# Kernel tuning notes

Measured on AMD Instinct MI355X. Metric: run time of the kernel, lower is better.

## Reference

```python
import math
import jax, jax.numpy as jnp
import numpy as np

DIM = 1280
NUM_HEADS = 16
HEAD_DIM = DIM // NUM_HEADS  # 80
N_SEG = 8
SEG_LEN = 1024
TOTAL = N_SEG * SEG_LEN  # 8192


def setup_inputs() -> dict:
    key = jax.random.key(0)
    ks = jax.random.split(key, 6)
    hidden_states = jax.random.normal(ks[0], (TOTAL, DIM), dtype=jnp.float32)
    # equal-length packed segments (8 images x 1024 patches)
    cu_seqlens = jnp.arange(N_SEG + 1, dtype=jnp.int32) * SEG_LEN
    rotary_pos_emb = jax.random.uniform(ks[1], (TOTAL, HEAD_DIM // 2), dtype=jnp.float32) * (2.0 * math.pi)
    s = 0.02
    qkv_w = jax.random.normal(ks[2], (DIM, 3 * DIM), dtype=jnp.float32) * s
    qkv_b = jnp.zeros((3 * DIM,), dtype=jnp.float32)
    proj_w = jax.random.normal(ks[3], (DIM, DIM), dtype=jnp.float32) * s
    proj_b = jnp.zeros((DIM,), dtype=jnp.float32)
    return {
        "hidden_states": hidden_states,
        "rotary_pos_emb": rotary_pos_emb,
        "qkv_w": qkv_w,
        "qkv_b": qkv_b,
        "proj_w": proj_w,
        "proj_b": proj_b,
        "cu_seqlens": cu_seqlens,
    }


def _rotate_half(x):
    d = x.shape[-1] // 2
    return jnp.concatenate([-x[..., d:], x[..., :d]], axis=-1)


def _apply_rope(t, freqs):
    # t: [S, H, D] ; freqs: [S, D/2]
    orig = t.dtype
    tf = t.astype(jnp.float32)
    cos = jnp.tile(jnp.cos(freqs), (1, 2))[:, None, :].astype(jnp.float32)  # [S,1,D]
    sin = jnp.tile(jnp.sin(freqs), (1, 2))[:, None, :].astype(jnp.float32)
    return (tf * cos + _rotate_half(tf) * sin).astype(orig)


def reference(hidden_states, rotary_pos_emb, qkv_w, qkv_b, proj_w, proj_b, cu_seqlens):
    S, dim = hidden_states.shape
    H, D = NUM_HEADS, HEAD_DIM
    n_seg = cu_seqlens.shape[0] - 1  # static
    L = S // n_seg  # equal-length segments

    qkv = hidden_states @ qkv_w + qkv_b            # [S, 3*dim]
    qkv = qkv.reshape(S, 3, H, D)
    q, k, v = qkv[:, 0], qkv[:, 1], qkv[:, 2]      # [S, H, D]

    q = _apply_rope(q, rotary_pos_emb)
    k = _apply_rope(k, rotary_pos_emb)

    # block-diagonal (per-segment) attention, vectorized over segments
    qs = q.reshape(n_seg, L, H, D).transpose(0, 2, 1, 3)  # [G,H,L,D]
    ks = k.reshape(n_seg, L, H, D).transpose(0, 2, 1, 3)
    vs = v.reshape(n_seg, L, H, D).transpose(0, 2, 1, 3)

    scale = 1.0 / math.sqrt(D)
    scores = jnp.einsum("ghld,ghmd->ghlm", qs, ks) * scale       # [G,H,L,L]
    probs = jax.nn.softmax(scores.astype(jnp.float32), axis=-1).astype(qs.dtype)
    out = jnp.einsum("ghlm,ghmd->ghld", probs, vs)               # [G,H,L,D]
    out = out.transpose(0, 2, 1, 3).reshape(S, H * D)            # [S, dim]
    return out @ proj_w + proj_b
```

## Files before the change

kernel.cpp:

```cpp
#include <hip/hip_runtime.h>
#include <hip/hip_bf16.h>
#include <math.h>

#define DIM 1280
#define NHEADS 16
#define HD 80
#define HDP 96
#define NSEG 8
#define SEGLEN 1024
#define TOTAL (NSEG*SEGLEN)

typedef unsigned short u16;
typedef __attribute__((ext_vector_type(8))) short bf16x8;
typedef __attribute__((ext_vector_type(4))) float f32x4;

#define QSCALE 0.16129841766598387f

__device__ __forceinline__ u16 f2b(float f) {
    union { float f; unsigned int i; } v; v.f = f;
    unsigned int x = v.i;
    unsigned int r = x + 0x7FFFu + ((x >> 16) & 1u);
    return (u16)(r >> 16);
}
__device__ __forceinline__ float b2f(u16 u) {
    union { unsigned int i; float f; } v; v.i = ((unsigned int)u) << 16;
    return v.f;
}
__device__ __forceinline__ void gload16(const u16* g, u16* l) {
    __builtin_amdgcn_global_load_lds(
        (const __attribute__((address_space(1))) unsigned int*)g,
        (__attribute__((address_space(3))) unsigned int*)l, 16, 0, 0);
}
__device__ __forceinline__ unsigned int cvt_pk_bf16(float lo, float hi) {
    unsigned int r;
    asm("v_cvt_pk_bf16_f32 %0, %1, %2" : "=v"(r) : "v"(lo), "v"(hi));
    return r;
}

__global__ __launch_bounds__(256) void cvt_f32_bf16(const float* __restrict__ in,
                                                    u16* __restrict__ out, int n4) {
    int i = blockIdx.x * 256 + threadIdx.x;
    if (i >= n4) return;
    float4 a = ((const float4*)in)[i];
    u16 o[4] = { f2b(a.x), f2b(a.y), f2b(a.z), f2b(a.w) };
    *(ulong1*)&out[i*4] = *(ulong1*)o;
}

__global__ __launch_bounds__(256) void cvtT_w(const float* __restrict__ in,
                                              u16* __restrict__ out, int K, int N) {
    __shared__ float t[32][33];
    const int kb = blockIdx.x * 32, nb = blockIdx.y * 32;
    const int tx = threadIdx.x & 31, ty = threadIdx.x >> 5;
    #pragma unroll
    for (int i = 0; i < 4; ++i) {
        int r = i*8 + ty;
        t[r][tx] = in[(size_t)(kb + r)*N + nb + tx];
    }
    __syncthreads();
    #pragma unroll
    for (int i = 0; i < 4; ++i) {
        int n = i*8 + ty;
        out[(size_t)(nb + n)*K + kb + tx] = f2b(t[tx][n]);
    }
}

__global__ __launch_bounds__(256) void ctab_build(const float* __restrict__ rp,
                                                  float2* __restrict__ cs) {
    int i = blockIdx.x * 256 + threadIdx.x;
    if (i >= TOTAL*40) return;
    float s, c;
    sincosf(rp[i], &s, &c);
    cs[i] = make_float2(c, s);
}

template<int MODE>
__global__ __launch_bounds__(512, 2) void gemm8p(
    const u16* __restrict__ A, const u16* __restrict__ BT,
    const float* __restrict__ bias,
    float* __restrict__ Cf, u16* __restrict__ qo, u16* __restrict__ ko,
    u16* __restrict__ vo, int M, int N, int K, int nbx)
{
    __shared__ u16 sA[2][256*64];
    __shared__ u16 sB[2][256*64];

    const int tid = threadIdx.x;
    const int w = tid >> 6, l = tid & 63;
    const int lq = l & 15, lg = l >> 4;
    const int wm = w >> 2, wn = w & 3;

    const int nwg = gridDim.x;
    const int q8 = nwg >> 3;
    const int id = blockIdx.x;
    const int id2 = (id & 7) * q8 + (id >> 3);
    const int bx = id2 % nbx, by = id2 / nbx;
    const int brow = by * 256, bcol = bx * 256;

    const int rlo  = w*8 + (l >> 3);
    const int srcc = (l & 7) ^ ((l >> 3) & 7);
    const size_t aBase = (size_t)(brow + rlo)*K + srcc*8;
    const size_t bBase = (size_t)(bcol + rlo)*K + srcc*8;

    const int cx0 = (0 + lg) ^ (lq & 7);
    const int cx1 = (4 + lg) ^ (lq & 7);

    f32x4 acc[8][4] = {};
    const int NT = K >> 6;

    u16* cA = &sA[0][0]; u16* cB = &sB[0][0];
    u16* nA = &sA[1][0]; u16* nB = &sB[1][0];

    #pragma unroll
    for (int ci = 0; ci < 4; ++ci) {
        gload16(A  + aBase + (size_t)(ci*64)*K, &cA[(ci*512 + w*64)*8]);
        gload16(BT + bBase + (size_t)(ci*64)*K, &cB[(ci*512 + w*64)*8]);
    }
    asm volatile("s_waitcnt vmcnt(0)" ::: "memory");
    __builtin_amdgcn_s_barrier();

    for (int t = 0; t < NT; ++t) {
        const bool pf = (t + 1 < NT);
        const int kb = (t + 1) << 6;
        bf16x8 af[4], bf[4];

        if (pf) {
            #pragma unroll
            for (int ci = 0; ci < 4; ++ci) {
                gload16(A  + aBase + (size_t)(ci*64)*K + kb, &nA[(ci*512 + w*64)*8]);
                gload16(BT + bBase + (size_t)(ci*64)*K + kb, &nB[(ci*512 + w*64)*8]);
            }
        }

        #pragma unroll
        for (int n = 0; n < 4; ++n)
            bf[n] = *(const bf16x8*)&cB[(wn*64 + n*16 + lq)*64 + cx0*8];
        #pragma unroll
        for (int mi = 0; mi < 4; ++mi)
            af[mi] = *(const bf16x8*)&cA[(wm*128 + mi*16 + lq)*64 + cx0*8];
        __builtin_amdgcn_s_barrier();
        __builtin_amdgcn_s_setprio(1);
        #pragma unroll
        for (int mi = 0; mi < 4; ++mi)
            #pragma unroll
            for (int n = 0; n < 4; ++n)
                acc[mi][n] = __builtin_amdgcn_mfma_f32_16x16x32_bf16(af[mi], bf[n], acc[mi][n], 0, 0, 0);
        __builtin_amdgcn_s_setprio(0);
        __builtin_amdgcn_s_barrier();

        #pragma unroll
        for (int mi = 0; mi < 4; ++mi)
            af[mi] = *(const bf16x8*)&cA[(wm*128 + 64 + mi*16 + lq)*64 + cx0*8];
        __builtin_amdgcn_s_barrier();
        __builtin_amdgcn_s_setprio(1);
        #pragma unroll
        for (int mi = 0; mi < 4; ++mi)
            #pragma unroll
            for (int n = 0; n < 4; ++n)
                acc[4+mi][n] = __builtin_amdgcn_mfma_f32_16x16x32_bf16(af[mi], bf[n], acc[4+mi][n], 0, 0, 0);
        __builtin_amdgcn_s_setprio(0);
        __builtin_amdgcn_s_barrier();

        #pragma unroll
        for (int n = 0; n < 4; ++n)
            bf[n] = *(const bf16x8*)&cB[(wn*64 + n*16 + lq)*64 + cx1*8];
        #pragma unroll
        for (int mi = 0; mi < 4; ++mi)
            af[mi] = *(const bf16x8*)&cA[(wm*128 + mi*16 + lq)*64 + cx1*8];
        __builtin_amdgcn_s_barrier();
        __builtin_amdgcn_s_setprio(1);
        #pragma unroll
        for (int mi = 0; mi < 4; ++mi)
            #pragma unroll
            for (int n = 0; n < 4; ++n)
                acc[mi][n] = __builtin_amdgcn_mfma_f32_16x16x32_bf16(af[mi], bf[n], acc[mi][n], 0, 0, 0);
        __builtin_amdgcn_s_setprio(0);
        __builtin_amdgcn_s_barrier();

        #pragma unroll
        for (int mi = 0; mi < 4; ++mi)
            af[mi] = *(const bf16x8*)&cA[(wm*128 + 64 + mi*16 + lq)*64 + cx1*8];
        __builtin_amdgcn_s_barrier();
        __builtin_amdgcn_s_setprio(1);
        #pragma unroll
        for (int mi = 0; mi < 4; ++mi)
            #pragma unroll
            for (int n = 0; n < 4; ++n)
                acc[4+mi][n] = __builtin_amdgcn_mfma_f32_16x16x32_bf16(af[mi], bf[n], acc[4+mi][n], 0, 0, 0);
        __builtin_amdgcn_s_setprio(0);
        if (pf) asm volatile("s_waitcnt vmcnt(0)" ::: "memory");
        __builtin_amdgcn_s_barrier();

        u16* tA = cA; cA = nA; nA = tA;
        u16* tB = cB; cB = nB; nB = tB;
    }

    #pragma unroll
    for (int mf = 0; mf < 8; ++mf) {
        #pragma unroll
        for (int n = 0; n < 4; ++n) {
            const int col = bcol + wn*64 + n*16 + lq;
            const float bv = bias[col];
            #pragma unroll
            for (int r = 0; r < 4; ++r) {
                const int row = brow + wm*128 + mf*16 + lg*4 + r;
                float val = acc[mf][n][r] + bv;
                if (MODE == 0) {
                    Cf[(size_t)row*N + col] = val;
                } else {
                    int part = col / DIM, rem = col - part*DIM;
                    int hh = rem / HD, dd = rem - hh*HD;
                    int g = row >> 10, ll = row & 1023;
                    size_t tok = (size_t)((g*NHEADS + hh)*SEGLEN + ll);
                    if      (part == 0) qo[tok*HDP + dd] = f2b(val * QSCALE);
                    else if (part == 1) ko[tok*HDP + dd] = f2b(val);
                    else                vo[tok*HD  + dd] = f2b(val);
                }
            }
        }
    }
}

__global__ __launch_bounds__(256) void rope_pad2(u16* __restrict__ qb, u16* __restrict__ kb,
                                                 const float2* __restrict__ cs)
{
    int idx = blockIdx.x * 256 + threadIdx.x;
    int l = idx & 1023, h = (idx >> 10) & 15, g = idx >> 14;
    size_t base = ((size_t)((g*NHEADS + h)*SEGLEN + l)) * HDP;
    const float2* c0 = cs + (size_t)(g*SEGLEN + l) * 40;
    #pragma unroll
    for (int p = 0; p < 5; ++p) {
        float cv[8], sv[8];
        #pragma unroll
        for (int j2 = 0; j2 < 4; ++j2) {
            float4 f = ((const float4*)(c0 + p*8))[j2];
            cv[j2*2] = f.x; sv[j2*2] = f.y; cv[j2*2+1] = f.z; sv[j2*2+1] = f.w;
        }
        bf16x8 qlo = *(const bf16x8*)&qb[base + p*8];
        bf16x8 qhi = *(const bf16x8*)&qb[base + 40 + p*8];
        bf16x8 klo = *(const bf16x8*)&kb[base + p*8];
        bf16x8 khi = *(const bf16x8*)&kb[base + 40 + p*8];
        bf16x8 qlo2, qhi2, klo2, khi2;
        #pragma unroll
        for (int j = 0; j < 8; ++j) {
            float a  = b2f((u16)qlo[j]), b  = b2f((u16)qhi[j]);
            qlo2[j] = (short)f2b(a*cv[j]  - b*sv[j]);
            qhi2[j] = (short)f2b(b*cv[j]  + a*sv[j]);
            float ka = b2f((u16)klo[j]), kb2 = b2f((u16)khi[j]);
            klo2[j] = (short)f2b(ka*cv[j] - kb2*sv[j]);
            khi2[j] = (short)f2b(kb2*cv[j] + ka*sv[j]);
        }
        *(bf16x8*)&qb[base + p*8]      = qlo2;
        *(bf16x8*)&qb[base + 40 + p*8] = qhi2;
        *(bf16x8*)&kb[base + p*8]      = klo2;
        *(bf16x8*)&kb[base + 40 + p*8] = khi2;
    }
    bf16x8 z = {};
    *(bf16x8*)&qb[base + 80] = z; *(bf16x8*)&qb[base + 88] = z;
    *(bf16x8*)&kb[base + 80] = z; *(bf16x8*)&kb[base + 88] = z;
}

__global__ __launch_bounds__(256) void transpose_v(const u16* __restrict__ v,
                                                   u16* __restrict__ vt)
{
    __shared__ u16 sT[64][82];
    const int gh = blockIdx.y;
    const int st = blockIdx.x;
    const u16* src = v  + (size_t)gh*SEGLEN*HD + (size_t)st*64*HD;
    u16*       dst = vt + (size_t)gh*HD*SEGLEN + (size_t)st*64;
    const int tid = threadIdx.x;
    #pragma unroll
    for (int p = 0; p < 20; ++p) {
        int e = p*256 + tid;
        int r = e / 80, c = e - r*80;
        sT[r][c] = src[r*HD + c];
    }
    __syncthreads();
    #pragma unroll
    for (int p = 0; p < 20; ++p) {
        int e = p*256 + tid;
        int dd = e >> 6, s = e & 63;
        dst[(size_t)dd*SEGLEN + s] = sT[s][dd];
    }
}

__global__ __launch_bounds__(256) void attn_mfma(
    const u16* __restrict__ qb, const u16* __restrict__ kb,
    const u16* __restrict__ vt, u16* __restrict__ ob)
{
    const int qt = blockIdx.x;
    const int h  = blockIdx.y;
    const int g  = blockIdx.z;

    __shared__ u16 sK[64*HDP];
    __shared__ u16 sVT[80][72];
    __shared__ u16 sP[4][16][72];

    const int tid = threadIdx.x;
    const int w = tid >> 6, l = tid & 63;
    const int lq = l & 15, lg = l >> 4;

    const size_t gh = (size_t)(g*NHEADS + h);
    const u16* Qg  = qb + gh*SEGLEN*HDP + (size_t)qt*64*HDP;
    const u16* Kg  = kb + gh*SEGLEN*HDP;
    const u16* VTg = vt + gh*HD*SEGLEN;

    const int sig_l = l ^ ((l >> 3) & 7);
    int srow[3], scc[3];
    #pragma unroll
    for (int i = 0; i < 3; ++i) {
        int gi = (i*4 + w)*64 + sig_l;
        srow[i] = gi / 12;
        scc[i]  = gi % 12;
    }

    bf16x8 qf[3];
    #pragma unroll
    for (int s = 0; s < 3; ++s)
        qf[s] = *(const bf16x8*)(Qg + (size_t)(w*16 + lq)*HDP + s*32 + lg*8);

    float m = -1e30f, lse = 0.f;
    f32x4 Oc[5] = {};

    for (int kt = 0; kt < 16; ++kt) {
        __syncthreads();
        #pragma unroll
        for (int i = 0; i < 3; ++i)
            gload16(Kg + (size_t)(kt*64 + srow[i])*HDP + scc[i]*8, &sK[(i*4 + w)*512]);
        #pragma unroll
        for (int p = 0; p < 3; ++p) {
            int c = p*256 + tid;
            if (c < 640) {
                int dd = c >> 3, s8 = (c & 7)*8;
                *(bf16x8*)&sVT[dd][s8] =
                    *(const bf16x8*)(VTg + (size_t)dd*SEGLEN + kt*64 + s8);
            }
        }
        __syncthreads();

        f32x4 sf[4];
        #pragma unroll
        for (int fi = 0; fi < 4; ++fi) {
            f32x4 c = {0.f, 0.f, 0.f, 0.f};
            #pragma unroll
            for (int s = 0; s < 3; ++s) {
                int flat = (fi*16 + lq)*12 + s*4 + lg;
                int c6 = flat & 63;
                int lc = (flat & ~63) | (c6 ^ ((c6 >> 3) & 7));
                bf16x8 a = *(const bf16x8*)&sK[lc*8];
                c = __builtin_amdgcn_mfma_f32_16x16x32_bf16(a, qf[s], c, 0, 0, 0);
            }
            sf[fi] = c;
        }

        float sv[4][4];
        float rm = -1e30f;
        #pragma unroll
        for (int fi = 0; fi < 4; ++fi)
            #pragma unroll
            for (int r = 0; r < 4; ++r) {
                float x = sf[fi][r];
                sv[fi][r] = x;
                rm = fmaxf(rm, x);
            }
        rm = fmaxf(rm, __shfl_xor(rm, 16, 64));
        rm = fmaxf(rm, __shfl_xor(rm, 32, 64));

        if (__all(rm <= m + 8.0f)) {
            float psum = 0.f;
            #pragma unroll
            for (int fi = 0; fi < 4; ++fi)
                #pragma unroll
                for (int r = 0; r < 4; ++r) {
                    float p = exp2f(sv[fi][r] - m);
                    sv[fi][r] = p;
                    psum += p;
                }
            psum += __shfl_xor(psum, 16, 64);
            psum += __shfl_xor(psum, 32, 64);
            lse += psum;
        } else {
            float mnew = fmaxf(m, rm);
            float alpha = exp2f(m - mnew);
            float psum = 0.f;
            #pragma unroll
            for (int fi = 0; fi < 4; ++fi)
                #pragma unroll
                for (int r = 0; r < 4; ++r) {
                    float p = exp2f(sv[fi][r] - mnew);
                    sv[fi][r] = p;
                    psum += p;
                }
            psum += __shfl_xor(psum, 16, 64);
            psum += __shfl_xor(psum, 32, 64);
            lse = lse * alpha + psum;
            m = mnew;
            float a0 = __shfl(alpha, lg*4 + 0, 64);
            float a1 = __shfl(alpha, lg*4 + 1, 64);
            float a2 = __shfl(alpha, lg*4 + 2, 64);
            float a3 = __shfl(alpha, lg*4 + 3, 64);
            #pragma unroll
            for (int n = 0; n < 5; ++n) {
                Oc[n][0] *= a0; Oc[n][1] *= a1; Oc[n][2] *= a2; Oc[n][3] *= a3;
            }
        }

        #pragma unroll
        for (int fi = 0; fi < 4; ++fi) {
            uint2 val;
            val.x = cvt_pk_bf16(sv[fi][0], sv[fi][1]);
            val.y = cvt_pk_bf16(sv[fi][2], sv[fi][3]);
            *(uint2*)&sP[w][lq][fi*16 + lg*4] = val;
        }

        #pragma unroll
        for (int ks = 0; ks < 2; ++ks) {
            bf16x8 pa = *(const bf16x8*)&sP[w][lq][ks*32 + lg*8];
            #pragma unroll
            for (int n = 0; n < 5; ++n) {
                bf16x8 vb = *(const bf16x8*)&sVT[n*16 + lq][ks*32 + lg*8];
                Oc[n] = __builtin_amdgcn_mfma_f32_16x16x32_bf16(pa, vb, Oc[n], 0, 0, 0);
            }
        }
    }

    float inv = 1.f / lse;
    float i0 = __shfl(inv, lg*4 + 0, 64);
    float i1 = __shfl(inv, lg*4 + 1, 64);
    float i2 = __shfl(inv, lg*4 + 2, 64);
    float i3 = __shfl(inv, lg*4 + 3, 64);
    const float iv[4] = { i0, i1, i2, i3 };
    #pragma unroll
    for (int n = 0; n < 5; ++n) {
        #pragma unroll
        for (int r = 0; r < 4; ++r) {
            int tok = g*SEGLEN + qt*64 + w*16 + lg*4 + r;
            int col = h*HD + n*16 + lq;
            ob[(size_t)tok*DIM + col] = f2b(Oc[n][r] * iv[r]);
        }
    }
}

extern "C" void kernel_launch(void* const* d_in, const int* in_sizes, int n_in,
                              void* d_out, int out_size, void* d_ws, size_t ws_size,
                              hipStream_t stream) {
    const float* hs     = (const float*)d_in[0];
    const float* rope   = (const float*)d_in[1];
    const float* qkv_w  = (const float*)d_in[2];
    const float* qkv_b  = (const float*)d_in[3];
    const float* proj_w = (const float*)d_in[4];
    const float* proj_b = (const float*)d_in[5];

    char* ws = (char*)d_ws;
    u16* hsb    = (u16*)(ws);
    u16* wqkvt  = (u16*)(ws + 20971520);
    u16* wprojt = (u16*)(ws + 30801920);
    u16* qpad   = (u16*)(ws + 34078720);
    u16* kpad   = (u16*)(ws + 59244544);
    u16* vbuf   = (u16*)(ws + 84410368);
    u16* vtb    = (u16*)(ws + 105381888);
    u16* obb    = (u16*)(ws + 126353408);
    float2* ctab = (float2*)(ws + 126353408);

    cvt_f32_bf16<<<(TOTAL*DIM/4 + 255)/256, 256, 0, stream>>>(hs, hsb, TOTAL*DIM/4);
    cvtT_w<<<dim3(DIM/32, 3*DIM/32), 256, 0, stream>>>(qkv_w, wqkvt, DIM, 3*DIM);
    cvtT_w<<<dim3(DIM/32, DIM/32), 256, 0, stream>>>(proj_w, wprojt, DIM, DIM);
    ctab_build<<<(TOTAL*40 + 255)/256, 256, 0, stream>>>(rope, ctab);

    gemm8p<1><<<dim3((3*DIM/256) * (TOTAL/256)), 512, 0, stream>>>(
        hsb, wqkvt, qkv_b, nullptr, qpad, kpad, vbuf, TOTAL, 3*DIM, DIM, 3*DIM/256);

    rope_pad2<<<NSEG*NHEADS*SEGLEN/256, 256, 0, stream>>>(qpad, kpad, ctab);

    transpose_v<<<dim3(SEGLEN/64, NSEG*NHEADS), 256, 0, stream>>>(vbuf, vtb);

    attn_mfma<<<dim3(SEGLEN/64, NHEADS, NSEG), 256, 0, stream>>>(qpad, kpad, vtb, obb);

    gemm8p<0><<<dim3((DIM/256) * (TOTAL/256)), 512, 0, stream>>>(
        obb, wprojt, proj_b, (float*)d_out, nullptr, nullptr, nullptr, TOTAL, DIM, DIM, DIM/256);
}
```

Baseline: 478.8 us.

## Restructure GEMM pipeline, fuse V transpose, widen rope threads, double attention query tile

The GEMM now uses a depth-2 prefetch with partial vmcnt waits and far fewer barriers per K step, with K fixed at compile time. The QKV epilogue writes V directly in transposed layout, which removes the separate transpose kernel and its buffer. The rope kernel splits each row across six threads for more parallelism. Attention processes 128 queries per block (32 per wave), so each K/V tile loaded into shared memory is reused twice, at the cost of higher register pressure and half as many blocks.

Result: faster. 434.0 us (-9.4%).

```diff
diff --git a/kernel.cpp b/kernel.cpp
--- a/kernel.cpp
+++ b/kernel.cpp
@@ -74,12 +74,14 @@
 }
 
 template<int MODE>
-__global__ __launch_bounds__(512, 2) void gemm8p(
+__global__ __launch_bounds__(512, 2) void gemm_cv(
     const u16* __restrict__ A, const u16* __restrict__ BT,
     const float* __restrict__ bias,
     float* __restrict__ Cf, u16* __restrict__ qo, u16* __restrict__ ko,
-    u16* __restrict__ vo, int M, int N, int K, int nbx)
+    u16* __restrict__ vo, int M, int N, int nbx)
 {
+    const int K = 1280;
+    const int NT = 20;
     __shared__ u16 sA[2][256*64];
     __shared__ u16 sB[2][256*64];
 
@@ -104,7 +106,6 @@
     const int cx1 = (4 + lg) ^ (lq & 7);
 
     f32x4 acc[8][4] = {};
-    const int NT = K >> 6;
 
     u16* cA = &sA[0][0]; u16* cB = &sB[0][0];
     u16* nA = &sA[1][0]; u16* nB = &sB[1][0];
@@ -114,81 +115,51 @@
         gload16(A  + aBase + (size_t)(ci*64)*K, &cA[(ci*512 + w*64)*8]);
         gload16(BT + bBase + (size_t)(ci*64)*K, &cB[(ci*512 + w*64)*8]);
     }
-    asm volatile("s_waitcnt vmcnt(0)" ::: "memory");
-    __builtin_amdgcn_s_barrier();
-
+    #pragma unroll
+    for (int ci = 0; ci < 4; ++ci) {
+        gload16(A  + aBase + (size_t)(ci*64)*K + 64, &nA[(ci*512 + w*64)*8]);
+        gload16(BT + bBase + (size_t)(ci*64)*K + 64, &nB[(ci*512 + w*64)*8]);
+    }
+
+    #pragma unroll 2
     for (int t = 0; t < NT; ++t) {
-        const bool pf = (t + 1 < NT);
-        const int kb = (t + 1) << 6;
-        bf16x8 af[4], bf[4];
-
-        if (pf) {
+        if (t < NT - 1) asm volatile("s_waitcnt vmcnt(8)" ::: "memory");
+        else            asm volatile("s_waitcnt vmcnt(0)" ::: "memory");
+        __builtin_amdgcn_s_barrier();
+
+        #pragma unroll
+        for (int kh = 0; kh < 2; ++kh) {
+            const int cx = kh ? cx1 : cx0;
+            bf16x8 bf[4];
+            #pragma unroll
+            for (int n = 0; n < 4; ++n)
+                bf[n] = *(const bf16x8*)&cB[(wn*64 + n*16 + lq)*64 + cx*8];
+            #pragma unroll
+            for (int mh = 0; mh < 2; ++mh) {
+                bf16x8 af[4];
+                #pragma unroll
+                for (int mi = 0; mi < 4; ++mi)
+                    af[mi] = *(const bf16x8*)&cA[(wm*128 + mh*64 + mi*16 + lq)*64 + cx*8];
+                __builtin_amdgcn_s_setprio(1);
+                #pragma unroll
+                for (int mi = 0; mi < 4; ++mi)
+                    #pragma unroll
+                    for (int n = 0; n < 4; ++n)
+                        acc[mh*4 + mi][n] = __builtin_amdgcn_mfma_f32_16x16x32_bf16(
+                            af[mi], bf[n], acc[mh*4 + mi][n], 0, 0, 0);
+                __builtin_amdgcn_s_setprio(0);
+            }
+        }
+        __builtin_amdgcn_s_barrier();
+
+        if (t + 2 < NT) {
+            const size_t kb2 = (size_t)(t + 2) * 64;
             #pragma unroll
             for (int ci = 0; ci < 4; ++ci) {
-                gload16(A  + aBase + (size_t)(ci*64)*K + kb, &nA[(ci*512 + w*64)*8]);
-                gload16(BT + bBase + (size_t)(ci*64)*K + kb, &nB[(ci*512 + w*64)*8]);
-            }
-        }
-
-        #pragma unroll
-        for (int n = 0; n < 4; ++n)
-            bf[n] = *(const bf16x8*)&cB[(wn*64 + n*16 + lq)*64 + cx0*8];
-        #pragma unroll
-        for (int mi = 0; mi < 4; ++mi)
-            af[mi] = *(const bf16x8*)&cA[(wm*128 + mi*16 + lq)*64 + cx0*8];
-        __builtin_amdgcn_s_barrier();
-        __builtin_amdgcn_s_setprio(1);
-        #pragma unroll
-        for (int mi = 0; mi < 4; ++mi)
-            #pragma unroll
-            for (int n = 0; n < 4; ++n)
-                acc[mi][n] = __builtin_amdgcn_mfma_f32_16x16x32_bf16(af[mi], bf[n], acc[mi][n], 0, 0, 0);
-        __builtin_amdgcn_s_setprio(0);
-        __builtin_amdgcn_s_barrier();
-
-        #pragma unroll
-        for (int mi = 0; mi < 4; ++mi)
-            af[mi] = *(const bf16x8*)&cA[(wm*128 + 64 + mi*16 + lq)*64 + cx0*8];
-        __builtin_amdgcn_s_barrier();
-        __builtin_amdgcn_s_setprio(1);
-        #pragma unroll
-        for (int mi = 0; mi < 4; ++mi)
-            #pragma unroll
-            for (int n = 0; n < 4; ++n)
-                acc[4+mi][n] = __builtin_amdgcn_mfma_f32_16x16x32_bf16(af[mi], bf[n], acc[4+mi][n], 0, 0, 0);
-        __builtin_amdgcn_s_setprio(0);
-        __builtin_amdgcn_s_barrier();
-
-        #pragma unroll
-        for (int n = 0; n < 4; ++n)
-            bf[n] = *(const bf16x8*)&cB[(wn*64 + n*16 + lq)*64 + cx1*8];
-        #pragma unroll
-        for (int mi = 0; mi < 4; ++mi)
-            af[mi] = *(const bf16x8*)&cA[(wm*128 + mi*16 + lq)*64 + cx1*8];
-        __builtin_amdgcn_s_barrier();
-        __builtin_amdgcn_s_setprio(1);
-        #pragma unroll
-        for (int mi = 0; mi < 4; ++mi)
-            #pragma unroll
-            for (int n = 0; n < 4; ++n)
-                acc[mi][n] = __builtin_amdgcn_mfma_f32_16x16x32_bf16(af[mi], bf[n], acc[mi][n], 0, 0, 0);
-        __builtin_amdgcn_s_setprio(0);
-        __builtin_amdgcn_s_barrier();
-
-        #pragma unroll
-        for (int mi = 0; mi < 4; ++mi)
-            af[mi] = *(const bf16x8*)&cA[(wm*128 + 64 + mi*16 + lq)*64 + cx1*8];
-        __builtin_amdgcn_s_barrier();
-        __builtin_amdgcn_s_setprio(1);
-        #pragma unroll
-        for (int mi = 0; mi < 4; ++mi)
-            #pragma unroll
-            for (int n = 0; n < 4; ++n)
-                acc[4+mi][n] = __builtin_amdgcn_mfma_f32_16x16x32_bf16(af[mi], bf[n], acc[4+mi][n], 0, 0, 0);
-        __builtin_amdgcn_s_setprio(0);
-        if (pf) asm volatile("s_waitcnt vmcnt(0)" ::: "memory");
-        __builtin_amdgcn_s_barrier();
-
+                gload16(A  + aBase + (size_t)(ci*64)*K + kb2, &cA[(ci*512 + w*64)*8]);
+                gload16(BT + bBase + (size_t)(ci*64)*K + kb2, &cB[(ci*512 + w*64)*8]);
+            }
+        }
         u16* tA = cA; cA = nA; nA = tA;
         u16* tB = cB; cB = nB; nB = tB;
     }
@@ -212,73 +183,102 @@
                     size_t tok = (size_t)((g*NHEADS + hh)*SEGLEN + ll);
                     if      (part == 0) qo[tok*HDP + dd] = f2b(val * QSCALE);
                     else if (part == 1) ko[tok*HDP + dd] = f2b(val);
-                    else                vo[tok*HD  + dd] = f2b(val);
+                    else    vo[((size_t)(g*NHEADS + hh)*HD + dd)*SEGLEN + ll] = f2b(val);
                 }
             }
         }
     }
 }
 
-__global__ __launch_bounds__(256) void rope_pad2(u16* __restrict__ qb, u16* __restrict__ kb,
+__global__ __launch_bounds__(256) void rope_pad3(u16* __restrict__ qb, u16* __restrict__ kb,
                                                  const float2* __restrict__ cs)
 {
     int idx = blockIdx.x * 256 + threadIdx.x;
-    int l = idx & 1023, h = (idx >> 10) & 15, g = idx >> 14;
-    size_t base = ((size_t)((g*NHEADS + h)*SEGLEN + l)) * HDP;
-    const float2* c0 = cs + (size_t)(g*SEGLEN + l) * 40;
-    #pragma unroll
-    for (int p = 0; p < 5; ++p) {
-        float cv[8], sv[8];
-        #pragma unroll
-        for (int j2 = 0; j2 < 4; ++j2) {
-            float4 f = ((const float4*)(c0 + p*8))[j2];
-            cv[j2*2] = f.x; sv[j2*2] = f.y; cv[j2*2+1] = f.z; sv[j2*2+1] = f.w;
-        }
-        bf16x8 qlo = *(const bf16x8*)&qb[base + p*8];
-        bf16x8 qhi = *(const bf16x8*)&qb[base + 40 + p*8];
-        bf16x8 klo = *(const bf16x8*)&kb[base + p*8];
-        bf16x8 khi = *(const bf16x8*)&kb[base + 40 + p*8];
-        bf16x8 qlo2, qhi2, klo2, khi2;
-        #pragma unroll
-        for (int j = 0; j < 8; ++j) {
-            float a  = b2f((u16)qlo[j]), b  = b2f((u16)qhi[j]);
-            qlo2[j] = (short)f2b(a*cv[j]  - b*sv[j]);
-            qhi2[j] = (short)f2b(b*cv[j]  + a*sv[j]);
-            float ka = b2f((u16)klo[j]), kb2 = b2f((u16)khi[j]);
-            klo2[j] = (short)f2b(ka*cv[j] - kb2*sv[j]);
-            khi2[j] = (short)f2b(kb2*cv[j] + ka*sv[j]);
-        }
-        *(bf16x8*)&qb[base + p*8]      = qlo2;
-        *(bf16x8*)&qb[base + 40 + p*8] = qhi2;
-        *(bf16x8*)&kb[base + p*8]      = klo2;
-        *(bf16x8*)&kb[base + 40 + p*8] = khi2;
-    }
-    bf16x8 z = {};
-    *(bf16x8*)&qb[base + 80] = z; *(bf16x8*)&qb[base + 88] = z;
-    *(bf16x8*)&kb[base + 80] = z; *(bf16x8*)&kb[base + 88] = z;
-}
-
-__global__ __launch_bounds__(256) void transpose_v(const u16* __restrict__ v,
-                                                   u16* __restrict__ vt)
+    int row = idx / 6, task = idx - row*6;
+    size_t base = (size_t)row * HDP;
+    if (task == 5) {
+        bf16x8 z = {};
+        *(bf16x8*)&qb[base + 80] = z; *(bf16x8*)&qb[base + 88] = z;
+        *(bf16x8*)&kb[base + 80] = z; *(bf16x8*)&kb[base + 88] = z;
+        return;
+    }
+    const int p = task;
+    int l = row & 1023, g = row >> 14;
+    const float2* c0 = cs + ((size_t)((g << 10) | l))*40 + p*8;
+    float cv[8], sv[8];
+    #pragma unroll
+    for (int j2 = 0; j2 < 4; ++j2) {
+        float4 f = ((const float4*)c0)[j2];
+        cv[j2*2] = f.x; sv[j2*2] = f.y; cv[j2*2+1] = f.z; sv[j2*2+1] = f.w;
+    }
+    bf16x8 qlo = *(const bf16x8*)&qb[base + p*8];
+    bf16x8 qhi = *(const bf16x8*)&qb[base + 40 + p*8];
+    bf16x8 klo = *(const bf16x8*)&kb[base + p*8];
+    bf16x8 khi = *(const bf16x8*)&kb[base + 40 + p*8];
+    bf16x8 qlo2, qhi2, klo2, khi2;
+    #pragma unroll
+    for (int j = 0; j < 8; ++j) {
+        float a  = b2f((u16)qlo[j]), b  = b2f((u16)qhi[j]);
+        qlo2[j] = (short)f2b(a*cv[j]  - b*sv[j]);
+        qhi2[j] = (short)f2b(b*cv[j]  + a*sv[j]);
+        float ka = b2f((u16)klo[j]), kb2 = b2f((u16)khi[j]);
+        klo2[j] = (short)f2b(ka*cv[j] - kb2*sv[j]);
+        khi2[j] = (short)f2b(kb2*cv[j] + ka*sv[j]);
+    }
+    *(bf16x8*)&qb[base + p*8]      = qlo2;
+    *(bf16x8*)&qb[base + 40 + p*8] = qhi2;
+    *(bf16x8*)&kb[base + p*8]      = klo2;
+    *(bf16x8*)&kb[base + 40 + p*8] = khi2;
+}
+
+__device__ __forceinline__ void sm_update(float sv[4][4], float& m, float& lse,
+                                          f32x4* Oc, const int lg)
 {
-    __shared__ u16 sT[64][82];
-    const int gh = blockIdx.y;
-    const int st = blockIdx.x;
-    const u16* src = v  + (size_t)gh*SEGLEN*HD + (size_t)st*64*HD;
-    u16*       dst = vt + (size_t)gh*HD*SEGLEN + (size_t)st*64;
-    const int tid = threadIdx.x;
-    #pragma unroll
-    for (int p = 0; p < 20; ++p) {
-        int e = p*256 + tid;
-        int r = e / 80, c = e - r*80;
-        sT[r][c] = src[r*HD + c];
-    }
-    __syncthreads();
-    #pragma unroll
-    for (int p = 0; p < 20; ++p) {
-        int e = p*256 + tid;
-        int dd = e >> 6, s = e & 63;
-        dst[(size_t)dd*SEGLEN + s] = sT[s][dd];
+    float rm = -1e30f;
+    #pragma unroll
+    for (int fi = 0; fi < 4; ++fi)
+        #pragma unroll
+        for (int r = 0; r < 4; ++r) rm = fmaxf(rm, sv[fi][r]);
+    rm = fmaxf(rm, __shfl_xor(rm, 16, 64));
+    rm = fmaxf(rm, __shfl_xor(rm, 32, 64));
+
+    if (__all(rm <= m + 8.0f)) {
+        float psum = 0.f;
+        #pragma unroll
+        for (int fi = 0; fi < 4; ++fi)
+            #pragma unroll
+            for (int r = 0; r < 4; ++r) {
+                float p = exp2f(sv[fi][r] - m);
+                sv[fi][r] = p;
+                psum += p;
+            }
+        psum += __shfl_xor(psum, 16, 64);
+        psum += __shfl_xor(psum, 32, 64);
+        lse += psum;
+    } else {
+        float mnew = fmaxf(m, rm);
+        float alpha = exp2f(m - mnew);
+        float psum = 0.f;
+        #pragma unroll
+        for (int fi = 0; fi < 4; ++fi)
+            #pragma unroll
+            for (int r = 0; r < 4; ++r) {
+                float p = exp2f(sv[fi][r] - mnew);
+                sv[fi][r] = p;
+                psum += p;
+            }
+        psum += __shfl_xor(psum, 16, 64);
+        psum += __shfl_xor(psum, 32, 64);
+        lse = lse * alpha + psum;
+        m = mnew;
+        float a0 = __shfl(alpha, lg*4 + 0, 64);
+        float a1 = __shfl(alpha, lg*4 + 1, 64);
+        float a2 = __shfl(alpha, lg*4 + 2, 64);
+        float a3 = __shfl(alpha, lg*4 + 3, 64);
+        #pragma unroll
+        for (int n = 0; n < 5; ++n) {
+            Oc[n][0] *= a0; Oc[n][1] *= a1; Oc[n][2] *= a2; Oc[n][3] *= a3;
+        }
     }
 }
 
@@ -292,39 +292,35 @@
 
     __shared__ u16 sK[64*HDP];
     __shared__ u16 sVT[80][72];
-    __shared__ u16 sP[4][16][72];
+    __shared__ u16 sP[4][32][72];
 
     const int tid = threadIdx.x;
     const int w = tid >> 6, l = tid & 63;
     const int lq = l & 15, lg = l >> 4;
 
     const size_t gh = (size_t)(g*NHEADS + h);
-    const u16* Qg  = qb + gh*SEGLEN*HDP + (size_t)qt*64*HDP;
+    const u16* Qg  = qb + gh*SEGLEN*HDP + (size_t)qt*128*HDP;
     const u16* Kg  = kb + gh*SEGLEN*HDP;
     const u16* VTg = vt + gh*HD*SEGLEN;
 
-    const int sig_l = l ^ ((l >> 3) & 7);
-    int srow[3], scc[3];
-    #pragma unroll
-    for (int i = 0; i < 3; ++i) {
-        int gi = (i*4 + w)*64 + sig_l;
-        srow[i] = gi / 12;
-        scc[i]  = gi % 12;
-    }
-
-    bf16x8 qf[3];
-    #pragma unroll
-    for (int s = 0; s < 3; ++s)
-        qf[s] = *(const bf16x8*)(Qg + (size_t)(w*16 + lq)*HDP + s*32 + lg*8);
-
-    float m = -1e30f, lse = 0.f;
-    f32x4 Oc[5] = {};
+    bf16x8 qf[2][3];
+    #pragma unroll
+    for (int qs = 0; qs < 2; ++qs)
+        #pragma unroll
+        for (int s = 0; s < 3; ++s)
+            qf[qs][s] = *(const bf16x8*)(Qg + (size_t)(w*32 + qs*16 + lq)*HDP + s*32 + lg*8);
+
+    float m0 = -1e30f, lse0 = 0.f, m1 = -1e30f, lse1 = 0.f;
+    f32x4 Oc0[5] = {}, Oc1[5] = {};
 
     for (int kt = 0; kt < 16; ++kt) {
         __syncthreads();
         #pragma unroll
-        for (int i = 0; i < 3; ++i)
-            gload16(Kg + (size_t)(kt*64 + srow[i])*HDP + scc[i]*8, &sK[(i*4 + w)*512]);
+        for (int i = 0; i < 3; ++i) {
+            int o = (i*4 + w)*1024 + l*16;
+            int row = o / 192, cc = (o % 192) >> 1;
+            gload16(Kg + (size_t)(kt*64 + row)*HDP + cc, &sK[(i*4 + w)*512]);
+        }
         #pragma unroll
         for (int p = 0; p < 3; ++p) {
             int c = p*256 + tid;
@@ -336,105 +332,63 @@
         }
         __syncthreads();
 
-        f32x4 sf[4];
-        #pragma unroll
-        for (int fi = 0; fi < 4; ++fi) {
-            f32x4 c = {0.f, 0.f, 0.f, 0.f};
-            #pragma unroll
-            for (int s = 0; s < 3; ++s) {
-                int flat = (fi*16 + lq)*12 + s*4 + lg;
-                int c6 = flat & 63;
-                int lc = (flat & ~63) | (c6 ^ ((c6 >> 3) & 7));
-                bf16x8 a = *(const bf16x8*)&sK[lc*8];
-                c = __builtin_amdgcn_mfma_f32_16x16x32_bf16(a, qf[s], c, 0, 0, 0);
-            }
-            sf[fi] = c;
-        }
-
-        float sv[4][4];
-        float rm = -1e30f;
-        #pragma unroll
-        for (int fi = 0; fi < 4; ++fi)
+        #pragma unroll
+        for (int qs = 0; qs < 2; ++qs) {
+            float sv[4][4];
+            #pragma unroll
+            for (int fi = 0; fi < 4; ++fi) {
+                f32x4 c = {0.f, 0.f, 0.f, 0.f};
+                #pragma unroll
+                for (int s = 0; s < 3; ++s) {
+                    bf16x8 a = *(const bf16x8*)&sK[(fi*16 + lq)*HDP + s*32 + lg*8];
+                    c = __builtin_amdgcn_mfma_f32_16x16x32_bf16(a, qf[qs][s], c, 0, 0, 0);
+                }
+                #pragma unroll
+                for (int r = 0; r < 4; ++r) sv[fi][r] = c[r];
+            }
+
+            if (qs == 0) sm_update(sv, m0, lse0, Oc0, lg);
+            else         sm_update(sv, m1, lse1, Oc1, lg);
+
+            #pragma unroll
+            for (int fi = 0; fi < 4; ++fi) {
+                uint2 val;
+                val.x = cvt_pk_bf16(sv[fi][0], sv[fi][1]);
+                val.y = cvt_pk_bf16(sv[fi][2], sv[fi][3]);
+                *(uint2*)&sP[w][qs*16 + lq][fi*16 + lg*4] = val;
+            }
+
+            f32x4* Oc = (qs == 0) ? Oc0 : Oc1;
+            #pragma unroll
+            for (int ks = 0; ks < 2; ++ks) {
+                bf16x8 pa = *(const bf16x8*)&sP[w][qs*16 + lq][ks*32 + lg*8];
+                #pragma unroll
+                for (int n = 0; n < 5; ++n) {
+                    bf16x8 vb = *(const bf16x8*)&sVT[n*16 + lq][ks*32 + lg*8];
+                    Oc[n] = __builtin_amdgcn_mfma_f32_16x16x32_bf16(pa, vb, Oc[n], 0, 0, 0);
+                }
+            }
+        }
+    }
+
+    #pragma unroll
+    for (int qs = 0; qs < 2; ++qs) {
+        float lse = (qs == 0) ? lse0 : lse1;
+        const f32x4* Oc = (qs == 0) ? Oc0 : Oc1;
+        float inv = 1.f / lse;
+        float i0 = __shfl(inv, lg*4 + 0, 64);
+        float i1 = __shfl(inv, lg*4 + 1, 64);
+        float i2 = __shfl(inv, lg*4 + 2, 64);
+        float i3 = __shfl(inv, lg*4 + 3, 64);
+        const float iv[4] = { i0, i1, i2, i3 };
+        #pragma unroll
+        for (int n = 0; n < 5; ++n) {
             #pragma unroll
             for (int r = 0; r < 4; ++r) {
-                float x = sf[fi][r];
-                sv[fi][r] = x;
-                rm = fmaxf(rm, x);
-            }
-        rm = fmaxf(rm, __shfl_xor(rm, 16, 64));
-        rm = fmaxf(rm, __shfl_xor(rm, 32, 64));
-
-        if (__all(rm <= m + 8.0f)) {
-            float psum = 0.f;
-            #pragma unroll
-            for (int fi = 0; fi < 4; ++fi)
-                #pragma unroll
-                for (int r = 0; r < 4; ++r) {
-                    float p = exp2f(sv[fi][r] - m);
-                    sv[fi][r] = p;
-                    psum += p;
-                }
-            psum += __shfl_xor(psum, 16, 64);
-            psum += __shfl_xor(psum, 32, 64);
-            lse += psum;
-        } else {
-            float mnew = fmaxf(m, rm);
-            float alpha = exp2f(m - mnew);
-            float psum = 0.f;
-            #pragma unroll
-            for (int fi = 0; fi < 4; ++fi)
-                #pragma unroll
-                for (int r = 0; r < 4; ++r) {
-                    float p = exp2f(sv[fi][r] - mnew);
-                    sv[fi][r] = p;
-                    psum += p;
-                }
-            psum += __shfl_xor(psum, 16, 64);
-            psum += __shfl_xor(psum, 32, 64);
-            lse = lse * alpha + psum;
-            m = mnew;
-            float a0 = __shfl(alpha, lg*4 + 0, 64);
-            float a1 = __shfl(alpha, lg*4 + 1, 64);
-            float a2 = __shfl(alpha, lg*4 + 2, 64);
-            float a3 = __shfl(alpha, lg*4 + 3, 64);
-            #pragma unroll
-            for (int n = 0; n < 5; ++n) {
-                Oc[n][0] *= a0; Oc[n][1] *= a1; Oc[n][2] *= a2; Oc[n][3] *= a3;
-            }
-        }
-
-        #pragma unroll
-        for (int fi = 0; fi < 4; ++fi) {
-            uint2 val;
-            val.x = cvt_pk_bf16(sv[fi][0], sv[fi][1]);
-            val.y = cvt_pk_bf16(sv[fi][2], sv[fi][3]);
-            *(uint2*)&sP[w][lq][fi*16 + lg*4] = val;
-        }
-
-        #pragma unroll
-        for (int ks = 0; ks < 2; ++ks) {
-            bf16x8 pa = *(const bf16x8*)&sP[w][lq][ks*32 + lg*8];
-            #pragma unroll
-            for (int n = 0; n < 5; ++n) {
-                bf16x8 vb = *(const bf16x8*)&sVT[n*16 + lq][ks*32 + lg*8];
-                Oc[n] = __builtin_amdgcn_mfma_f32_16x16x32_bf16(pa, vb, Oc[n], 0, 0, 0);
-            }
-        }
-    }
-
-    float inv = 1.f / lse;
-    float i0 = __shfl(inv, lg*4 + 0, 64);
-    float i1 = __shfl(inv, lg*4 + 1, 64);
-    float i2 = __shfl(inv, lg*4 + 2, 64);
-    float i3 = __shfl(inv, lg*4 + 3, 64);
-    const float iv[4] = { i0, i1, i2, i3 };
-    #pragma unroll
-    for (int n = 0; n < 5; ++n) {
-        #pragma unroll
-        for (int r = 0; r < 4; ++r) {
-            int tok = g*SEGLEN + qt*64 + w*16 + lg*4 + r;
-            int col = h*HD + n*16 + lq;
-            ob[(size_t)tok*DIM + col] = f2b(Oc[n][r] * iv[r]);
+                int tok = g*SEGLEN + qt*128 + w*32 + qs*16 + lg*4 + r;
+                int col = h*HD + n*16 + lq;
+                ob[(size_t)tok*DIM + col] = f2b(Oc[n][r] * iv[r]);
+            }
         }
     }
 }
@@ -455,25 +409,22 @@
     u16* wprojt = (u16*)(ws + 30801920);
     u16* qpad   = (u16*)(ws + 34078720);
     u16* kpad   = (u16*)(ws + 59244544);
-    u16* vbuf   = (u16*)(ws + 84410368);
-    u16* vtb    = (u16*)(ws + 105381888);
-    u16* obb    = (u16*)(ws + 126353408);
-    float2* ctab = (float2*)(ws + 126353408);
+    u16* vtb    = (u16*)(ws + 84410368);
+    u16* obb    = (u16*)(ws + 105381888);
+    float2* ctab = (float2*)(ws + 105381888);
 
     cvt_f32_bf16<<<(TOTAL*DIM/4 + 255)/256, 256, 0, stream>>>(hs, hsb, TOTAL*DIM/4);
     cvtT_w<<<dim3(DIM/32, 3*DIM/32), 256, 0, stream>>>(qkv_w, wqkvt, DIM, 3*DIM);
     cvtT_w<<<dim3(DIM/32, DIM/32), 256, 0, stream>>>(proj_w, wprojt, DIM, DIM);
     ctab_build<<<(TOTAL*40 + 255)/256, 256, 0, stream>>>(rope, ctab);
 
-    gemm8p<1><<<dim3((3*DIM/256) * (TOTAL/256)), 512, 0, stream>>>(
-        hsb, wqkvt, qkv_b, nullptr, qpad, kpad, vbuf, TOTAL, 3*DIM, DIM, 3*DIM/256);
-
-    rope_pad2<<<NSEG*NHEADS*SEGLEN/256, 256, 0, stream>>>(qpad, kpad, ctab);
-
-    transpose_v<<<dim3(SEGLEN/64, NSEG*NHEADS), 256, 0, stream>>>(vbuf, vtb);
-
-    attn_mfma<<<dim3(SEGLEN/64, NHEADS, NSEG), 256, 0, stream>>>(qpad, kpad, vtb, obb);
-
-    gemm8p<0><<<dim3((DIM/256) * (TOTAL/256)), 512, 0, stream>>>(
-        obb, wprojt, proj_b, (float*)d_out, nullptr, nullptr, nullptr, TOTAL, DIM, DIM, DIM/256);
-}
+    gemm_cv<1><<<dim3((3*DIM/256) * (TOTAL/256)), 512, 0, stream>>>(
+        hsb, wqkvt, qkv_b, nullptr, qpad, kpad, vtb, TOTAL, 3*DIM, 3*DIM/256);
+
+    rope_pad3<<<NSEG*NHEADS*SEGLEN*6/256, 256, 0, stream>>>(qpad, kpad, ctab);
+
+    attn_mfma<<<dim3(SEGLEN/128, NHEADS, NSEG), 256, 0, stream>>>(qpad, kpad, vtb, obb);
+
+    gemm_cv<0><<<dim3((DIM/256) * (TOTAL/256)), 512, 0, stream>>>(
+        obb, wprojt, proj_b, (float*)d_out, nullptr, nullptr, nullptr, TOTAL, DIM, DIM/256);
+}
```
